# Kernel tuning notes

Hardware: AMD Instinct MI355X
Metric: run time of the kernel (lower is better)

The kernel has to match this reference:

```python
import jax, jax.numpy as jnp
import numpy as np

K = 11
EPS = 1e-6


def _box_sum(a):
    # a: [B, H, W] -> KxK zero-padded local sum (equivalent to nn.Unfold padding=K//2 then sum)
    return jax.lax.reduce_window(a, 0.0, jax.lax.add,
                                 window_dimensions=(1, K, K),
                                 window_strides=(1, 1, 1),
                                 padding='SAME')


def setup_inputs() -> dict:
    key = jax.random.key(0)
    k1, k2 = jax.random.split(key)
    x = jax.random.normal(k1, (8, 3, 1024, 1024), dtype=jnp.float32)
    y = jax.random.normal(k2, (8, 3, 1024, 1024), dtype=jnp.float32)
    return {"x": x, "y": y}


def reference(x, y):
    # Channel-reduce first, then local KxK box sums (math-identical to the
    # unfold-based sum over (C, K, K) with zero padding).
    xx = _box_sum((x * x).sum(axis=1))   # [B, H, W]
    yy = _box_sum((y * y).sum(axis=1))
    xy = _box_sum((x * y).sum(axis=1))
    x_norm = jnp.sqrt(xx)
    y_norm = jnp.sqrt(yy)
    return xy / (x_norm * y_norm + EPS)
```

## Files before the change

### kernel.cpp

```cpp
#include <hip/hip_runtime.h>
#include <math.h>

#define NB 8
#define NC 3
#define NH 1024
#define NW 1024
#define KRAD 5
#define KSZ 11
#define EPS 1e-6f

#define TH 32
#define TW 64
#define HALO_H (TH + 2 * KRAD)
#define HALO_W (TW + 2 * KRAD)
#define PROW 76
#define NTHREADS 256

__global__ __launch_bounds__(NTHREADS)
void lcs_kernel(const float* __restrict__ x, const float* __restrict__ y,
                float* __restrict__ out) {
    __shared__ float P[3][HALO_H][PROW];
    __shared__ float Hs[HALO_H][TW];

    const int tid = threadIdx.x;
    const int w0 = blockIdx.x * TW;
    const int h0 = blockIdx.y * TH;
    const int b  = blockIdx.z;

    for (int i = tid; i < HALO_H * HALO_W; i += NTHREADS) {
        const int r  = i / HALO_W;
        const int cc = i - r * HALO_W;
        const int gh = h0 + r  - KRAD;
        const int gw = w0 + cc - KRAD;
        float sxx = 0.f, syy = 0.f, sxy = 0.f;
        if ((unsigned)gh < (unsigned)NH && (unsigned)gw < (unsigned)NW) {
            const size_t chan = (size_t)NH * NW;
            size_t base = (size_t)b * NC * chan + (size_t)gh * NW + gw;
            #pragma unroll
            for (int c = 0; c < NC; ++c) {
                const float xv = x[base + (size_t)c * chan];
                const float yv = y[base + (size_t)c * chan];
                sxx += xv * xv;
                syy += yv * yv;
                sxy += xv * yv;
            }
        }
        P[0][r][cc] = sxx;
        P[1][r][cc] = syy;
        P[2][r][cc] = sxy;
    }
    __syncthreads();

    const int c     = tid & (TW - 1);
    const int rbase = (tid >> 6) * 8;

    float acc[3][8];

    for (int p = 0; p < 3; ++p) {
        for (int u = tid; u < HALO_H * (TW / 4); u += NTHREADS) {
            const int r  = u >> 4;
            const int c4 = (u & 15) << 2;
            const float* row = &P[p][r][0];
            const float4 a0 = *(const float4*)(row + c4);
            const float4 a1 = *(const float4*)(row + c4 + 4);
            const float4 a2 = *(const float4*)(row + c4 + 8);
            const float4 a3 = *(const float4*)(row + c4 + 12);
            const float v0 = a0.x, v1 = a0.y, v2 = a0.z,  v3 = a0.w;
            const float v4 = a1.x, v5 = a1.y, v6 = a1.z,  v7 = a1.w;
            const float v8 = a2.x, v9 = a2.y, v10 = a2.z, v11 = a2.w;
            const float v12 = a3.x, v13 = a3.y;
            const float s0 = ((v0 + v1) + (v2 + v3)) + ((v4 + v5) + (v6 + v7))
                           + ((v8 + v9) + v10);
            const float s1 = s0 - v0 + v11;
            const float s2 = s1 - v1 + v12;
            const float s3 = s2 - v2 + v13;
            float4 o; o.x = s0; o.y = s1; o.z = s2; o.w = s3;
            *(float4*)(&Hs[r][c4]) = o;
        }
        __syncthreads();

        {
            float s = 0.f;
            #pragma unroll
            for (int d = 0; d < KSZ; ++d) s += Hs[rbase + d][c];
            acc[p][0] = s;
            #pragma unroll
            for (int j = 1; j < 8; ++j) {
                s += Hs[rbase + j + (KSZ - 1)][c] - Hs[rbase + j - 1][c];
                acc[p][j] = s;
            }
        }
        __syncthreads();
    }

    #pragma unroll
    for (int j = 0; j < 8; ++j) {
        const float xx = acc[0][j];
        const float yy = acc[1][j];
        const float xy = acc[2][j];
        const float denom = sqrtf(xx) * sqrtf(yy) + EPS;
        const size_t oidx = ((size_t)b * NH + (h0 + rbase + j)) * NW + (w0 + c);
        out[oidx] = xy / denom;
    }
}

extern "C" void kernel_launch(void* const* d_in, const int* in_sizes, int n_in,
                              void* d_out, int out_size, void* d_ws, size_t ws_size,
                              hipStream_t stream) {
    const float* x = (const float*)d_in[0];
    const float* y = (const float*)d_in[1];
    float* out = (float*)d_out;
    dim3 grid(NW / TW, NH / TH, NB);
    lcs_kernel<<<grid, NTHREADS, 0, stream>>>(x, y, out);
}
```

Baseline: 273.5 us.

## Fuse channel reduce with horizontal box sum using vectorized row loads

```diff
diff --git a/kernel.cpp b/kernel.cpp
--- a/kernel.cpp
+++ b/kernel.cpp
@@ -6,48 +6,76 @@
 #define NH 1024
 #define NW 1024
 #define KRAD 5
-#define KSZ 11
 #define EPS 1e-6f
 
 #define TH 32
 #define TW 64
 #define HALO_H (TH + 2 * KRAD)
-#define HALO_W (TW + 2 * KRAD)
-#define PROW 76
+#define HSTRIDE 65
 #define NTHREADS 256
+#define NUNITS (HALO_H * 8)
 
-__global__ __launch_bounds__(NTHREADS)
+__global__ __launch_bounds__(NTHREADS, 4)
 void lcs_kernel(const float* __restrict__ x, const float* __restrict__ y,
                 float* __restrict__ out) {
-    __shared__ float P[3][HALO_H][PROW];
-    __shared__ float Hs[HALO_H][TW];
+    __shared__ float Hs[3][HALO_H][HSTRIDE];
 
     const int tid = threadIdx.x;
     const int w0 = blockIdx.x * TW;
     const int h0 = blockIdx.y * TH;
     const int b  = blockIdx.z;
+    const size_t chan = (size_t)NH * NW;
+    const float* xb = x + (size_t)b * NC * chan;
+    const float* yb = y + (size_t)b * NC * chan;
 
-    for (int i = tid; i < HALO_H * HALO_W; i += NTHREADS) {
-        const int r  = i / HALO_W;
-        const int cc = i - r * HALO_W;
-        const int gh = h0 + r  - KRAD;
-        const int gw = w0 + cc - KRAD;
-        float sxx = 0.f, syy = 0.f, sxy = 0.f;
-        if ((unsigned)gh < (unsigned)NH && (unsigned)gw < (unsigned)NW) {
-            const size_t chan = (size_t)NH * NW;
-            size_t base = (size_t)b * NC * chan + (size_t)gh * NW + gw;
+    for (int u = tid; u < NUNITS; u += NTHREADS) {
+        const int row  = u >> 3;
+        const int colg = u & 7;
+        const int gh   = h0 + row - KRAD;
+        const int gw0  = w0 + colg * 8 - 8;
+
+        float hxx[8], hyy[8], hxy[8];
+        #pragma unroll
+        for (int j = 0; j < 8; ++j) { hxx[j] = 0.f; hyy[j] = 0.f; hxy[j] = 0.f; }
+
+        if ((unsigned)gh < (unsigned)NH) {
             #pragma unroll
             for (int c = 0; c < NC; ++c) {
-                const float xv = x[base + (size_t)c * chan];
-                const float yv = y[base + (size_t)c * chan];
-                sxx += xv * xv;
-                syy += yv * yv;
-                sxy += xv * yv;
+                const float* xr = xb + c * chan + (size_t)gh * NW;
+                const float* yr = yb + c * chan + (size_t)gh * NW;
+                float xv[24], yv[24];
+                #pragma unroll
+                for (int q = 0; q < 6; ++q) {
+                    const int cs = gw0 + 4 * q;
+                    const bool ok = (cs >= 0) && (cs <= NW - 4);
+                    float4 a  = ok ? *(const float4*)(xr + cs) : make_float4(0.f, 0.f, 0.f, 0.f);
+                    float4 bv = ok ? *(const float4*)(yr + cs) : make_float4(0.f, 0.f, 0.f, 0.f);
+                    xv[4*q] = a.x;  xv[4*q+1] = a.y;  xv[4*q+2] = a.z;  xv[4*q+3] = a.w;
+                    yv[4*q] = bv.x; yv[4*q+1] = bv.y; yv[4*q+2] = bv.z; yv[4*q+3] = bv.w;
+                }
+                float sxx = 0.f, syy = 0.f, sxy = 0.f;
+                #pragma unroll
+                for (int m = 3; m <= 13; ++m) {
+                    sxx += xv[m] * xv[m];
+                    syy += yv[m] * yv[m];
+                    sxy += xv[m] * yv[m];
+                }
+                hxx[0] += sxx; hyy[0] += syy; hxy[0] += sxy;
+                #pragma unroll
+                for (int j = 1; j < 8; ++j) {
+                    sxx += xv[j+13] * xv[j+13] - xv[j+2] * xv[j+2];
+                    syy += yv[j+13] * yv[j+13] - yv[j+2] * yv[j+2];
+                    sxy += xv[j+13] * yv[j+13] - xv[j+2] * yv[j+2];
+                    hxx[j] += sxx; hyy[j] += syy; hxy[j] += sxy;
+                }
             }
         }
-        P[0][r][cc] = sxx;
-        P[1][r][cc] = syy;
-        P[2][r][cc] = sxy;
+        #pragma unroll
+        for (int j = 0; j < 8; ++j) {
+            Hs[0][row][colg*8 + j] = hxx[j];
+            Hs[1][row][colg*8 + j] = hyy[j];
+            Hs[2][row][colg*8 + j] = hxy[j];
+        }
     }
     __syncthreads();
 
@@ -55,52 +83,24 @@
     const int rbase = (tid >> 6) * 8;
 
     float acc[3][8];
-
+    #pragma unroll
     for (int p = 0; p < 3; ++p) {
-        for (int u = tid; u < HALO_H * (TW / 4); u += NTHREADS) {
-            const int r  = u >> 4;
-            const int c4 = (u & 15) << 2;
-            const float* row = &P[p][r][0];
-            const float4 a0 = *(const float4*)(row + c4);
-            const float4 a1 = *(const float4*)(row + c4 + 4);
-            const float4 a2 = *(const float4*)(row + c4 + 8);
-            const float4 a3 = *(const float4*)(row + c4 + 12);
-            const float v0 = a0.x, v1 = a0.y, v2 = a0.z,  v3 = a0.w;
-            const float v4 = a1.x, v5 = a1.y, v6 = a1.z,  v7 = a1.w;
-            const float v8 = a2.x, v9 = a2.y, v10 = a2.z, v11 = a2.w;
-            const float v12 = a3.x, v13 = a3.y;
-            const float s0 = ((v0 + v1) + (v2 + v3)) + ((v4 + v5) + (v6 + v7))
-                           + ((v8 + v9) + v10);
-            const float s1 = s0 - v0 + v11;
-            const float s2 = s1 - v1 + v12;
-            const float s3 = s2 - v2 + v13;
-            float4 o; o.x = s0; o.y = s1; o.z = s2; o.w = s3;
-            *(float4*)(&Hs[r][c4]) = o;
-        }
-        __syncthreads();
-
-        {
-            float s = 0.f;
-            #pragma unroll
-            for (int d = 0; d < KSZ; ++d) s += Hs[rbase + d][c];
-            acc[p][0] = s;
-            #pragma unroll
-            for (int j = 1; j < 8; ++j) {
-                s += Hs[rbase + j + (KSZ - 1)][c] - Hs[rbase + j - 1][c];
-                acc[p][j] = s;
-            }
-        }
-        __syncthreads();
+        float h[18];
+        #pragma unroll
+        for (int d = 0; d < 18; ++d) h[d] = Hs[p][rbase + d][c];
+        float s = 0.f;
+        #pragma unroll
+        for (int d = 0; d < 11; ++d) s += h[d];
+        acc[p][0] = s;
+        #pragma unroll
+        for (int j = 1; j < 8; ++j) { s += h[j+10] - h[j-1]; acc[p][j] = s; }
     }
 
     #pragma unroll
     for (int j = 0; j < 8; ++j) {
-        const float xx = acc[0][j];
-        const float yy = acc[1][j];
-        const float xy = acc[2][j];
-        const float denom = sqrtf(xx) * sqrtf(yy) + EPS;
+        const float denom = sqrtf(acc[0][j]) * sqrtf(acc[1][j]) + EPS;
         const size_t oidx = ((size_t)b * NH + (h0 + rbase + j)) * NW + (w0 + c);
-        out[oidx] = xy / denom;
+        out[oidx] = acc[2][j] / denom;
     }
 }
 
```

Result: slower. 312.0 us (+14.1%).
